# Optimization experiments

Hardware: AMD Instinct MI355X
Metric: run time of the kernel (lower is better)

The kernel has to match this reference:

```python
import jax, jax.numpy as jnp
import numpy as np

NEG_SLOPE = 0.2  # PyG GATConv default negative_slope
EPS = 1e-16


def gat_conv(x, edge_index, W, att_src, att_dst, bias, heads, out_c, concat):
    """Faithful PyG GATConv forward (add_self_loops=True).
    x: [N, F_in], edge_index: [2, E] (row 0 = src, row 1 = dst),
    W: [heads*out_c, F_in], att_src/att_dst: [1, heads, out_c], bias: [out]
    """
    N = x.shape[0]
    loop = jnp.arange(N, dtype=edge_index.dtype)
    src = jnp.concatenate([edge_index[0], loop])
    dst = jnp.concatenate([edge_index[1], loop])

    h = (x @ W.T).reshape(N, heads, out_c)            # [N, H, C]
    a_src = jnp.sum(h * att_src, axis=-1)             # [N, H]
    a_dst = jnp.sum(h * att_dst, axis=-1)             # [N, H]

    e = jax.nn.leaky_relu(a_src[src] + a_dst[dst], NEG_SLOPE)   # [E+N, H]
    # numerically-stable segment softmax over incoming edges of dst
    m = jax.ops.segment_max(e, dst, num_segments=N)             # [N, H]
    p = jnp.exp(e - m[dst])
    denom = jax.ops.segment_sum(p, dst, num_segments=N)         # [N, H]
    alpha = p / (denom[dst] + EPS)                              # [E+N, H]

    out = jax.ops.segment_sum(h[src] * alpha[:, :, None], dst, num_segments=N)  # [N, H, C]
    out = out.reshape(N, heads * out_c) if concat else out.mean(axis=1)
    return out + bias


def setup_inputs() -> dict:
    key = jax.random.key(0)
    ks = jax.random.split(key, 11)
    N, E = 100_000, 1_600_000
    in_dim, hid, heads = 128, 64, 2
    s = 0.1
    x = jax.random.normal(ks[0], (N, in_dim), jnp.float32)
    edge_index_l2 = jax.random.randint(ks[1], (2, E), 0, N, dtype=jnp.int32)
    edge_index_l1 = jax.random.randint(ks[2], (2, E), 0, N, dtype=jnp.int32)
    # layer gat_l2: in_dim -> hid per head, heads=2, concat=True
    W2 = jax.random.normal(ks[3], (heads * hid, in_dim), jnp.float32) * s
    att_src2 = jax.random.normal(ks[4], (1, heads, hid), jnp.float32) * s
    att_dst2 = jax.random.normal(ks[5], (1, heads, hid), jnp.float32) * s
    b2 = jnp.zeros((heads * hid,), jnp.float32)
    # layer gat_l1: hid*heads -> hid, 1 head, concat=False
    W1 = jax.random.normal(ks[6], (hid, heads * hid), jnp.float32) * s
    att_src1 = jax.random.normal(ks[7], (1, 1, hid), jnp.float32) * s
    att_dst1 = jax.random.normal(ks[8], (1, 1, hid), jnp.float32) * s
    b1 = jnp.zeros((hid,), jnp.float32)
    return {
        "x": x,
        "edge_index_l1": edge_index_l1,
        "edge_index_l2": edge_index_l2,
        "W2": W2, "att_src2": att_src2, "att_dst2": att_dst2, "b2": b2,
        "W1": W1, "att_src1": att_src1, "att_dst1": att_dst1, "b1": b1,
    }


def reference(x, edge_index_l1, edge_index_l2, W2, att_src2, att_dst2, b2,
              W1, att_src1, att_dst1, b1):
    h = jax.nn.elu(gat_conv(x, edge_index_l2, W2, att_src2, att_dst2, b2,
                            heads=2, out_c=64, concat=True))    # [N, 128]
    h = jax.nn.elu(gat_conv(h, edge_index_l1, W1, att_src1, att_dst1, b1,
                            heads=1, out_c=64, concat=False))   # [N, 64]
    return h
```

## Files before the change

kernel.cpp:

```cpp
#include <hip/hip_runtime.h>
#include <hip/hip_bf16.h>
#include <math.h>

#define LRELU_SLOPE 0.2f
#define EPS 1e-16f
#define BUCK_SHIFT 8
#define BUCK_NODES 256
#define MAXBUCK 512

typedef __hip_bfloat16 bf16;
typedef __attribute__((ext_vector_type(8))) short bf16x8;
typedef __attribute__((ext_vector_type(4))) float f32x4;

__device__ inline float lrelu(float v) { return v > 0.f ? v : LRELU_SLOPE * v; }
__device__ inline float bflo(unsigned u) { return __uint_as_float(u << 16); }
__device__ inline float bfhi(unsigned u) { return __uint_as_float(u & 0xffff0000u); }
__device__ inline short f2bf(float f) {
  bf16 t = __float2bfloat16(f);
  return *reinterpret_cast<short*>(&t);
}
__device__ inline unsigned pack2(float lo, float hi) {
  return ((unsigned)(unsigned short)f2bf(hi) << 16) | (unsigned)(unsigned short)f2bf(lo);
}

__global__ void prep_kernel(const float* __restrict__ W2, unsigned short* __restrict__ Wb2,
                            const float* __restrict__ W1, unsigned short* __restrict__ Wb1,
                            int* __restrict__ gcur, int ngc) {
  int idx = blockIdx.x * blockDim.x + threadIdx.x;
  if (idx < ngc) gcur[idx] = 0;
  if (idx < 16384) {
    Wb2[idx] = (unsigned short)f2bf(W2[idx]);
  } else {
    int i = idx - 16384;
    if (i < 8192) Wb1[i] = (unsigned short)f2bf(W1[i]);
  }
}

template <int EPB>
__global__ __launch_bounds__(256) void partition_both_kernel(
    const int* __restrict__ ei2, int E2, int* __restrict__ gcur2, int* __restrict__ slab2,
    const int* __restrict__ ei1, int E1, int* __restrict__ gcur1, int* __restrict__ slab1,
    int cap, int nbuck, int nblk2) {
  __shared__ int cnt[MAXBUCK];
  __shared__ int sbase[MAXBUCK];
  const int tid = threadIdx.x;
  const bool l2 = (int)blockIdx.x < nblk2;
  const int bid = l2 ? blockIdx.x : blockIdx.x - nblk2;
  const int* ei = l2 ? ei2 : ei1;
  const int E = l2 ? E2 : E1;
  int* gcur = l2 ? gcur2 : gcur1;
  int* part = l2 ? slab2 : slab1;
  for (int t = tid; t < nbuck; t += 256) cnt[t] = 0;
  __syncthreads();
  const int e0 = bid * EPB;
  constexpr int KPT = EPB / 256;
  int sv[KPT], dv[KPT];
#pragma unroll
  for (int k = 0; k < KPT; k++) {
    int e = e0 + tid + k * 256;
    if (e < E) {
      sv[k] = ei[e];
      dv[k] = ei[E + e];
      atomicAdd(&cnt[dv[k] >> BUCK_SHIFT], 1);
    } else {
      dv[k] = -1;
    }
  }
  __syncthreads();
  for (int t = tid; t < nbuck; t += 256) {
    int c = cnt[t];
    if (c) sbase[t] = atomicAdd(&gcur[t], c);
    cnt[t] = 0;
  }
  __syncthreads();
#pragma unroll
  for (int k = 0; k < KPT; k++) {
    if (dv[k] >= 0) {
      int b = dv[k] >> BUCK_SHIFT;
      int pos = sbase[b] + atomicAdd(&cnt[b], 1);
      if (pos < cap) part[(size_t)b * cap + pos] = (sv[k] << 8) | (dv[k] & (BUCK_NODES - 1));
    }
  }
}

template <int H>
__global__ __launch_bounds__(256) void csr_build_kernel(
    int* __restrict__ slab, const int* __restrict__ gcur, int cap,
    const float* __restrict__ asrc, const float* __restrict__ adst, float* __restrict__ pcsr,
    int* __restrict__ rowbeg, int* __restrict__ rowend, int N) {
  extern __shared__ char smem[];
  int* s_sd = (int*)smem;
  int* hist = (int*)(s_sd + cap);
  int* histp = hist + 256;
  int* escanp = histp + 256;
  int* cur = escanp + 256;
  int* wtot = cur + 256;
  float* s_ad = (float*)(wtot + 4);

  const int b = blockIdx.x;
  const int tid = threadIdx.x;
  const int lane = tid & 63;
  const int wid = tid >> 6;
  const int nb0 = b << BUCK_SHIFT;
  const int nn = min(BUCK_NODES, N - nb0);
  const int cnt = min(gcur[b], cap - 7 * BUCK_NODES);
  const int B = b * cap;
  int* eidx = slab;

  hist[tid] = 0;
  cur[tid] = 0;
  for (int t = tid; t < nn * H; t += 256) s_ad[t] = adst[(size_t)nb0 * H + t];
  __syncthreads();
  for (int i = tid; i < cnt; i += 256) {
    int pr = slab[(size_t)B + i];
    s_sd[i] = pr;
    atomicAdd(&hist[pr & (BUCK_NODES - 1)], 1);
  }
  __syncthreads();
  const int h0 = hist[tid];
  const int hp = (h0 + 7) & ~7;
  histp[tid] = hp;
  int inc = hp;
#pragma unroll
  for (int off = 1; off < 64; off <<= 1) {
    int t = __shfl_up(inc, off);
    if (lane >= off) inc += t;
  }
  if (lane == 63) wtot[wid] = inc;
  __syncthreads();
  int base = 0;
  for (int w = 0; w < wid; w++) base += wtot[w];
  escanp[tid] = inc + base;
  if (tid < nn) {
    rowbeg[nb0 + tid] = B + inc + base - hp;
    rowend[nb0 + tid] = B + inc + base;
  }
  __syncthreads();
  for (int i = tid; i < cnt; i += 256) {
    int pr = s_sd[i];
    int d8 = pr & (BUCK_NODES - 1);
    int s = pr >> 8;
    int slot = B + (escanp[d8] - histp[d8]) + atomicAdd(&cur[d8], 1);
    eidx[slot] = s;
    if constexpr (H == 2) {
      float2 a = *(const float2*)&asrc[2 * (size_t)s];
      float2 ad = *(const float2*)&s_ad[2 * d8];
      float2 pv;
      pv.x = __expf(lrelu(a.x + ad.x));
      pv.y = __expf(lrelu(a.y + ad.y));
      *(float2*)&pcsr[2 * (size_t)slot] = pv;
    } else {
      pcsr[slot] = __expf(lrelu(asrc[s] + s_ad[d8]));
    }
  }
  if (tid < nn) {
    int pb = B + escanp[tid] - histp[tid];
    for (int k = h0; k < hp; k++) {
      eidx[pb + k] = nb0 + tid;
      if constexpr (H == 2) {
        *(float2*)&pcsr[2 * (size_t)(pb + k)] = make_float2(0.f, 0.f);
      } else {
        pcsr[pb + k] = 0.f;
      }
    }
  }
}

template <int M, int H, bool SPLIT, typename Tin>
__global__ __launch_bounds__(256) void gemm_att_mfma(
    const Tin* __restrict__ x, const unsigned short* __restrict__ Wb,
    const float* __restrict__ atts, const float* __restrict__ attd, bf16* __restrict__ h,
    float* __restrict__ asrc, float* __restrict__ adst, float* __restrict__ pself, int N) {
  constexpr int K = 128;
  constexpr int NF = M / 16;
  const int wid = threadIdx.x >> 6;
  const int lane = threadIdx.x & 63;
  const int r0 = blockIdx.x * 64 + wid * 16;
  if (r0 >= N) return;
  const int colb = lane & 15;
  const int kgrp = lane >> 4;
  const size_t arow = (size_t)min(r0 + colb, N - 1);

  f32x4 acc[NF];
#pragma unroll
  for (int f = 0; f < NF; f++) acc[f] = (f32x4){0.f, 0.f, 0.f, 0.f};

#pragma unroll
  for (int k0 = 0; k0 < K; k0 += 32) {
    const int kb = k0 + kgrp * 8;
    bf16x8 ahi, alo;
    if constexpr (SPLIT) {
      const float* xp = (const float*)x + arow * K + kb;
      float4 l0 = *(const float4*)xp;
      float4 l1 = *(const float4*)(xp + 4);
      float xv[8] = {l0.x, l0.y, l0.z, l0.w, l1.x, l1.y, l1.z, l1.w};
#pragma unroll
      for (int j = 0; j < 8; j++) {
        short hb = f2bf(xv[j]);
        ahi[j] = hb;
        float hf = __uint_as_float(((unsigned)(unsigned short)hb) << 16);
        alo[j] = f2bf(xv[j] - hf);
      }
    } else {
      ahi = *(const bf16x8*)((const unsigned short*)x + arow * K + kb);
    }
#pragma unroll
    for (int f = 0; f < NF; f++) {
      bf16x8 b = *(const bf16x8*)(Wb + (size_t)(f * 16 + colb) * K + kb);
      if constexpr (SPLIT)
        acc[f] = __builtin_amdgcn_mfma_f32_16x16x32_bf16(alo, b, acc[f], 0, 0, 0);
      acc[f] = __builtin_amdgcn_mfma_f32_16x16x32_bf16(ahi, b, acc[f], 0, 0, 0);
    }
  }

#pragma unroll
  for (int r = 0; r < 4; r++) {
    const int row = r0 + kgrp * 4 + r;
    const bool ok = row < N;
    float s0 = 0.f, d0 = 0.f, s1 = 0.f, d1 = 0.f;
#pragma unroll
    for (int f = 0; f < NF; f++) {
      float v = acc[f][r];
      int c = f * 16 + colb;
      if (ok) h[(size_t)row * M + c] = __float2bfloat16(v);
      float av = atts[c], dv = attd[c];
      if (H == 2 && f >= NF / 2) {
        s1 += v * av;
        d1 += v * dv;
      } else {
        s0 += v * av;
        d0 += v * dv;
      }
    }
#pragma unroll
    for (int off = 1; off < 16; off <<= 1) {
      s0 += __shfl_xor(s0, off);
      d0 += __shfl_xor(d0, off);
      if (H == 2) {
        s1 += __shfl_xor(s1, off);
        d1 += __shfl_xor(d1, off);
      }
    }
    if (ok && colb == 0) {
      if (H == 2) {
        asrc[2 * (size_t)row] = s0;
        asrc[2 * (size_t)row + 1] = s1;
        adst[2 * (size_t)row] = d0;
        adst[2 * (size_t)row + 1] = d1;
        *(float2*)&pself[2 * (size_t)row] =
            make_float2(__expf(lrelu(s0 + d0)), __expf(lrelu(s1 + d1)));
      } else {
        asrc[row] = s0;
        adst[row] = d0;
        pself[row] = __expf(lrelu(s0 + d0));
      }
    }
  }
}

__global__ void gather2_kernel(const bf16* __restrict__ h, const float* __restrict__ pself,
                               const int* __restrict__ rowbeg, const int* __restrict__ rowend,
                               const int* __restrict__ eidx, const float* __restrict__ pcsr,
                               const float* __restrict__ bias, bf16* __restrict__ outp, int N) {
  long long gt = (long long)blockIdx.x * blockDim.x + threadIdx.x;
  int n = (int)(gt >> 6);
  int lane = threadIdx.x & 63;
  if (n >= N) return;
  const int qw = lane >> 4;
  const int cl = lane & 15;
  const bool head0 = cl < 8;
  int start = rowbeg[n];
  int end = rowend[n];
  const float2 ps = *(const float2*)&pself[2 * (size_t)n];
  float g = qw ? 0.f : (head0 ? ps.x : ps.y);
  uint4 hv = *(const uint4*)&h[(size_t)n * 128 + 8 * cl];
  float den = g;
  float a0 = g * bflo(hv.x), a1 = g * bfhi(hv.x);
  float a2 = g * bflo(hv.y), a3 = g * bfhi(hv.y);
  float a4 = g * bflo(hv.z), a5 = g * bfhi(hv.z);
  float a6 = g * bflo(hv.w), a7 = g * bfhi(hv.w);
  for (int j = start + 4 * qw; j < end; j += 16) {
    int4 ia = *(const int4*)&eidx[j];
    float4 q0 = *(const float4*)&pcsr[2 * (size_t)j];
    float4 q1 = *(const float4*)&pcsr[2 * (size_t)j + 4];
    uint4 hA = *(const uint4*)&h[(size_t)ia.x * 128 + 8 * cl];
    uint4 hB = *(const uint4*)&h[(size_t)ia.y * 128 + 8 * cl];
    uint4 hC = *(const uint4*)&h[(size_t)ia.z * 128 + 8 * cl];
    uint4 hD = *(const uint4*)&h[(size_t)ia.w * 128 + 8 * cl];
    float pa = head0 ? q0.x : q0.y;
    float pb = head0 ? q0.z : q0.w;
    float pc = head0 ? q1.x : q1.y;
    float pd = head0 ? q1.z : q1.w;
    den += (pa + pb) + (pc + pd);
    a0 += (pa * bflo(hA.x) + pb * bflo(hB.x)) + (pc * bflo(hC.x) + pd * bflo(hD.x));
    a1 += (pa * bfhi(hA.x) + pb * bfhi(hB.x)) + (pc * bfhi(hC.x) + pd * bfhi(hD.x));
    a2 += (pa * bflo(hA.y) + pb * bflo(hB.y)) + (pc * bflo(hC.y) + pd * bflo(hD.y));
    a3 += (pa * bfhi(hA.y) + pb * bfhi(hB.y)) + (pc * bfhi(hC.y) + pd * bfhi(hD.y));
    a4 += (pa * bflo(hA.z) + pb * bflo(hB.z)) + (pc * bflo(hC.z) + pd * bflo(hD.z));
    a5 += (pa * bfhi(hA.z) + pb * bfhi(hB.z)) + (pc * bfhi(hC.z) + pd * bfhi(hD.z));
    a6 += (pa * bflo(hA.w) + pb * bflo(hB.w)) + (pc * bflo(hC.w) + pd * bflo(hD.w));
    a7 += (pa * bfhi(hA.w) + pb * bfhi(hB.w)) + (pc * bfhi(hC.w) + pd * bfhi(hD.w));
  }
#pragma unroll
  for (int off = 16; off <= 32; off <<= 1) {
    den += __shfl_xor(den, off);
    a0 += __shfl_xor(a0, off);
    a1 += __shfl_xor(a1, off);
    a2 += __shfl_xor(a2, off);
    a3 += __shfl_xor(a3, off);
    a4 += __shfl_xor(a4, off);
    a5 += __shfl_xor(a5, off);
    a6 += __shfl_xor(a6, off);
    a7 += __shfl_xor(a7, off);
  }
  if (qw == 0) {
    float rden = 1.f / (den + EPS);
    float4 bv0 = *(const float4*)&bias[8 * cl];
    float4 bv1 = *(const float4*)&bias[8 * cl + 4];
    float v0 = a0 * rden + bv0.x;
    float v1 = a1 * rden + bv0.y;
    float v2 = a2 * rden + bv0.z;
    float v3 = a3 * rden + bv0.w;
    float v4 = a4 * rden + bv1.x;
    float v5 = a5 * rden + bv1.y;
    float v6 = a6 * rden + bv1.z;
    float v7 = a7 * rden + bv1.w;
    v0 = v0 > 0.f ? v0 : expm1f(v0);
    v1 = v1 > 0.f ? v1 : expm1f(v1);
    v2 = v2 > 0.f ? v2 : expm1f(v2);
    v3 = v3 > 0.f ? v3 : expm1f(v3);
    v4 = v4 > 0.f ? v4 : expm1f(v4);
    v5 = v5 > 0.f ? v5 : expm1f(v5);
    v6 = v6 > 0.f ? v6 : expm1f(v6);
    v7 = v7 > 0.f ? v7 : expm1f(v7);
    uint4 o;
    o.x = pack2(v0, v1);
    o.y = pack2(v2, v3);
    o.z = pack2(v4, v5);
    o.w = pack2(v6, v7);
    *(uint4*)&outp[(size_t)n * 128 + 8 * cl] = o;
  }
}

__global__ void gather1_kernel(const bf16* __restrict__ h, const float* __restrict__ pself,
                               const int* __restrict__ rowbeg, const int* __restrict__ rowend,
                               const int* __restrict__ eidx, const float* __restrict__ pcsr,
                               const float* __restrict__ bias, float* __restrict__ outp, int N) {
  long long gt = (long long)blockIdx.x * blockDim.x + threadIdx.x;
  int n = (int)(gt >> 6);
  int lane = threadIdx.x & 63;
  if (n >= N) return;
  const int qw = lane >> 4;
  const int cl = lane & 15;
  int start = rowbeg[n];
  int end = rowend[n];
  uint2 hv = *(const uint2*)&h[(size_t)n * 64 + 4 * cl];
  float g = qw ? 0.f : pself[n];
  float den = g;
  float a0 = g * bflo(hv.x), a1 = g * bfhi(hv.x);
  float a2 = g * bflo(hv.y), a3 = g * bfhi(hv.y);
  for (int j = start + 4 * qw; j < end; j += 16) {
    int4 ia = *(const int4*)&eidx[j];
    float4 pv = *(const float4*)&pcsr[j];
    uint2 hA = *(const uint2*)&h[(size_t)ia.x * 64 + 4 * cl];
    uint2 hB = *(const uint2*)&h[(size_t)ia.y * 64 + 4 * cl];
    uint2 hC = *(const uint2*)&h[(size_t)ia.z * 64 + 4 * cl];
    uint2 hD = *(const uint2*)&h[(size_t)ia.w * 64 + 4 * cl];
    den += (pv.x + pv.y) + (pv.z + pv.w);
    a0 += (pv.x * bflo(hA.x) + pv.y * bflo(hB.x)) + (pv.z * bflo(hC.x) + pv.w * bflo(hD.x));
    a1 += (pv.x * bfhi(hA.x) + pv.y * bfhi(hB.x)) + (pv.z * bfhi(hC.x) + pv.w * bfhi(hD.x));
    a2 += (pv.x * bflo(hA.y) + pv.y * bflo(hB.y)) + (pv.z * bflo(hC.y) + pv.w * bflo(hD.y));
    a3 += (pv.x * bfhi(hA.y) + pv.y * bfhi(hB.y)) + (pv.z * bfhi(hC.y) + pv.w * bfhi(hD.y));
  }
#pragma unroll
  for (int off = 16; off <= 32; off <<= 1) {
    den += __shfl_xor(den, off);
    a0 += __shfl_xor(a0, off);
    a1 += __shfl_xor(a1, off);
    a2 += __shfl_xor(a2, off);
    a3 += __shfl_xor(a3, off);
  }
  if (qw == 0) {
    float rden = 1.f / (den + EPS);
    float4 bv = *(const float4*)&bias[4 * cl];
    float v0 = a0 * rden + bv.x;
    float v1 = a1 * rden + bv.y;
    float v2 = a2 * rden + bv.z;
    float v3 = a3 * rden + bv.w;
    v0 = v0 > 0.f ? v0 : expm1f(v0);
    v1 = v1 > 0.f ? v1 : expm1f(v1);
    v2 = v2 > 0.f ? v2 : expm1f(v2);
    v3 = v3 > 0.f ? v3 : expm1f(v3);
    *(float4*)&outp[(size_t)n * 64 + 4 * cl] = make_float4(v0, v1, v2, v3);
  }
}

extern "C" void kernel_launch(void* const* d_in, const int* in_sizes, int n_in,
                              void* d_out, int out_size, void* d_ws, size_t ws_size,
                              hipStream_t stream) {
  const float* x = (const float*)d_in[0];
  const int* ei1 = (const int*)d_in[1];
  const int* ei2 = (const int*)d_in[2];
  const float* W2 = (const float*)d_in[3];
  const float* as2 = (const float*)d_in[4];
  const float* ad2 = (const float*)d_in[5];
  const float* b2 = (const float*)d_in[6];
  const float* W1 = (const float*)d_in[7];
  const float* as1 = (const float*)d_in[8];
  const float* ad1 = (const float*)d_in[9];
  const float* b1 = (const float*)d_in[10];
  float* out = (float*)d_out;

  const int N = in_sizes[0] / 128;
  const int E1 = in_sizes[1] / 2;
  const int E2 = in_sizes[2] / 2;
  const int Emax = E1 > E2 ? E1 : E2;
  const size_t Ns = (size_t)N;

  const int nbuck = (N + BUCK_NODES - 1) / BUCK_NODES;
  int lam = (Emax + nbuck - 1) / nbuck;
  int cap = lam + (lam >> 2) + 2048;
  cap = (cap + 255) & ~(int)255;
  const size_t NC = (size_t)nbuck * cap;

  float* ws = (float*)d_ws;
  size_t o = 0;
  unsigned short* Wb2 = (unsigned short*)(ws + o); o += 8192;
  unsigned short* Wb1 = (unsigned short*)(ws + o); o += 4096;
  float* asrc2 = ws + o;  o += 2 * Ns;
  float* adst2 = ws + o;  o += 2 * Ns;
  float* pself2 = ws + o; o += 2 * Ns;
  float* asrc1 = ws + o;  o += Ns;
  float* adst1 = ws + o;  o += Ns;
  float* pself1 = ws + o; o += Ns;
  int* gcur2 = (int*)(ws + o);   o += (size_t)nbuck;
  int* gcur1 = (int*)(ws + o);   o += (size_t)nbuck;
  int* rowbeg2 = (int*)(ws + o); o += Ns;
  int* rowend2 = (int*)(ws + o); o += Ns;
  int* rowbeg1 = (int*)(ws + o); o += Ns;
  int* rowend1 = (int*)(ws + o); o += Ns;
  o = (o + 7) & ~(size_t)7;
  int* slab2 = (int*)(ws + o);   o += NC;
  int* slab1 = (int*)(ws + o);   o += NC;
  o = (o + 7) & ~(size_t)7;
  float* pcsr = ws + o;          o += 2 * NC;
  o = (o + 7) & ~(size_t)7;
  bf16* h2 = (bf16*)(ws + o);    o += 64 * Ns;
  bf16* h1 = h2;
  bf16* hin1 = (bf16*)(ws + o);  o += 64 * Ns;

  const size_t smem2 = (size_t)cap * 4 + 4 * 256 * 4 + 16 + 2 * 256 * 4 + 64;
  const size_t smem1 = (size_t)cap * 4 + 4 * 256 * 4 + 16 + 1 * 256 * 4 + 64;

  const int nblk2 = (E2 + 4095) / 4096;
  const int nblk1 = (E1 + 4095) / 4096;

  prep_kernel<<<(16384 + 8192 + 255) / 256, 256, 0, stream>>>(W2, Wb2, W1, Wb1, gcur2, 2 * nbuck);
  partition_both_kernel<4096><<<nblk2 + nblk1, 256, 0, stream>>>(
      ei2, E2, gcur2, slab2, ei1, E1, gcur1, slab1, cap, nbuck, nblk2);

  gemm_att_mfma<128, 2, true, float>
      <<<(N + 63) / 64, 256, 0, stream>>>(x, Wb2, as2, ad2, h2, asrc2, adst2, pself2, N);
  csr_build_kernel<2><<<nbuck, 256, smem2, stream>>>(slab2, gcur2, cap, asrc2, adst2, pcsr,
                                                     rowbeg2, rowend2, N);
  gather2_kernel<<<(N + 3) / 4, 256, 0, stream>>>(h2, pself2, rowbeg2, rowend2, slab2, pcsr,
                                                  b2, hin1, N);

  gemm_att_mfma<64, 1, false, bf16>
      <<<(N + 63) / 64, 256, 0, stream>>>(hin1, Wb1, as1, ad1, h1, asrc1, adst1, pself1, N);
  csr_build_kernel<1><<<nbuck, 256, smem1, stream>>>(slab1, gcur1, cap, asrc1, adst1, pcsr,
                                                     rowbeg1, rowend1, N);
  gather1_kernel<<<(N + 3) / 4, 256, 0, stream>>>(h1, pself1, rowbeg1, rowend1, slab1, pcsr,
                                                  b1, out, N);
}
```

Baseline: 315.2 us.

## Fuse CSR build with neighbor gather per bucket and halve bucket size

The separate CSR-build and gather kernels of each layer are merged into one kernel per bucket. After sorting its bucket's edges in shared memory, each block aggregates its own nodes, reading row offsets from the shared scan instead of global rowbeg/rowend arrays. Buckets shrink from 256 to 128 nodes, giving more blocks and a smaller per-bucket slab, and the capacity slack is tightened. This removes two launches and the rowbeg/rowend round trip, and keeps freshly written eidx/pcsr hot in cache. In exchange, gather parallelism drops to a few hundred blocks, each wave processing 32 nodes serially, which may weaken latency hiding for the random feature loads.

```diff
diff --git a/kernel.cpp b/kernel.cpp
--- a/kernel.cpp
+++ b/kernel.cpp
@@ -4,9 +4,9 @@
 
 #define LRELU_SLOPE 0.2f
 #define EPS 1e-16f
-#define BUCK_SHIFT 8
-#define BUCK_NODES 256
-#define MAXBUCK 512
+#define BUCK_SHIFT 7
+#define BUCK_NODES 128
+#define MAXBUCK 1024
 
 typedef __hip_bfloat16 bf16;
 typedef __attribute__((ext_vector_type(8))) short bf16x8;
@@ -78,90 +78,7 @@
     if (dv[k] >= 0) {
       int b = dv[k] >> BUCK_SHIFT;
       int pos = sbase[b] + atomicAdd(&cnt[b], 1);
-      if (pos < cap) part[(size_t)b * cap + pos] = (sv[k] << 8) | (dv[k] & (BUCK_NODES - 1));
-    }
-  }
-}
-
-template <int H>
-__global__ __launch_bounds__(256) void csr_build_kernel(
-    int* __restrict__ slab, const int* __restrict__ gcur, int cap,
-    const float* __restrict__ asrc, const float* __restrict__ adst, float* __restrict__ pcsr,
-    int* __restrict__ rowbeg, int* __restrict__ rowend, int N) {
-  extern __shared__ char smem[];
-  int* s_sd = (int*)smem;
-  int* hist = (int*)(s_sd + cap);
-  int* histp = hist + 256;
-  int* escanp = histp + 256;
-  int* cur = escanp + 256;
-  int* wtot = cur + 256;
-  float* s_ad = (float*)(wtot + 4);
-
-  const int b = blockIdx.x;
-  const int tid = threadIdx.x;
-  const int lane = tid & 63;
-  const int wid = tid >> 6;
-  const int nb0 = b << BUCK_SHIFT;
-  const int nn = min(BUCK_NODES, N - nb0);
-  const int cnt = min(gcur[b], cap - 7 * BUCK_NODES);
-  const int B = b * cap;
-  int* eidx = slab;
-
-  hist[tid] = 0;
-  cur[tid] = 0;
-  for (int t = tid; t < nn * H; t += 256) s_ad[t] = adst[(size_t)nb0 * H + t];
-  __syncthreads();
-  for (int i = tid; i < cnt; i += 256) {
-    int pr = slab[(size_t)B + i];
-    s_sd[i] = pr;
-    atomicAdd(&hist[pr & (BUCK_NODES - 1)], 1);
-  }
-  __syncthreads();
-  const int h0 = hist[tid];
-  const int hp = (h0 + 7) & ~7;
-  histp[tid] = hp;
-  int inc = hp;
-#pragma unroll
-  for (int off = 1; off < 64; off <<= 1) {
-    int t = __shfl_up(inc, off);
-    if (lane >= off) inc += t;
-  }
-  if (lane == 63) wtot[wid] = inc;
-  __syncthreads();
-  int base = 0;
-  for (int w = 0; w < wid; w++) base += wtot[w];
-  escanp[tid] = inc + base;
-  if (tid < nn) {
-    rowbeg[nb0 + tid] = B + inc + base - hp;
-    rowend[nb0 + tid] = B + inc + base;
-  }
-  __syncthreads();
-  for (int i = tid; i < cnt; i += 256) {
-    int pr = s_sd[i];
-    int d8 = pr & (BUCK_NODES - 1);
-    int s = pr >> 8;
-    int slot = B + (escanp[d8] - histp[d8]) + atomicAdd(&cur[d8], 1);
-    eidx[slot] = s;
-    if constexpr (H == 2) {
-      float2 a = *(const float2*)&asrc[2 * (size_t)s];
-      float2 ad = *(const float2*)&s_ad[2 * d8];
-      float2 pv;
-      pv.x = __expf(lrelu(a.x + ad.x));
-      pv.y = __expf(lrelu(a.y + ad.y));
-      *(float2*)&pcsr[2 * (size_t)slot] = pv;
-    } else {
-      pcsr[slot] = __expf(lrelu(asrc[s] + s_ad[d8]));
-    }
-  }
-  if (tid < nn) {
-    int pb = B + escanp[tid] - histp[tid];
-    for (int k = h0; k < hp; k++) {
-      eidx[pb + k] = nb0 + tid;
-      if constexpr (H == 2) {
-        *(float2*)&pcsr[2 * (size_t)(pb + k)] = make_float2(0.f, 0.f);
-      } else {
-        pcsr[pb + k] = 0.f;
-      }
+      if (pos < cap) part[(size_t)b * cap + pos] = (sv[k] << BUCK_SHIFT) | (dv[k] & (BUCK_NODES - 1));
     }
   }
 }
@@ -258,140 +175,209 @@
   }
 }
 
-__global__ void gather2_kernel(const bf16* __restrict__ h, const float* __restrict__ pself,
-                               const int* __restrict__ rowbeg, const int* __restrict__ rowend,
-                               const int* __restrict__ eidx, const float* __restrict__ pcsr,
-                               const float* __restrict__ bias, bf16* __restrict__ outp, int N) {
-  long long gt = (long long)blockIdx.x * blockDim.x + threadIdx.x;
-  int n = (int)(gt >> 6);
-  int lane = threadIdx.x & 63;
-  if (n >= N) return;
+template <int H, typename TOut>
+__global__ __launch_bounds__(256) void csr_gather_kernel(
+    int* __restrict__ slab, const int* __restrict__ gcur, int cap,
+    const float* __restrict__ asrc, const float* __restrict__ adst,
+    const float* __restrict__ pself, float* __restrict__ pcsr, const bf16* __restrict__ h,
+    const float* __restrict__ bias, TOut* __restrict__ outp, int N) {
+  extern __shared__ char smem[];
+  int* s_sd = (int*)smem;
+  int* hist = (int*)(s_sd + cap);
+  int* histp = hist + 256;
+  int* escanp = histp + 256;
+  int* cur = escanp + 256;
+  int* wtot = cur + 256;
+  float* s_ad = (float*)(wtot + 4);
+
+  const int b = blockIdx.x;
+  const int tid = threadIdx.x;
+  const int lane = tid & 63;
+  const int wid = tid >> 6;
+  const int nb0 = b << BUCK_SHIFT;
+  const int nn = min(BUCK_NODES, N - nb0);
+  const int cnt = min(gcur[b], cap - 7 * BUCK_NODES);
+  const int B = b * cap;
+  int* eidx = slab;
+
+  hist[tid] = 0;
+  cur[tid] = 0;
+  for (int t = tid; t < nn * H; t += 256) s_ad[t] = adst[(size_t)nb0 * H + t];
+  __syncthreads();
+  for (int i = tid; i < cnt; i += 256) {
+    int pr = slab[(size_t)B + i];
+    s_sd[i] = pr;
+    atomicAdd(&hist[pr & (BUCK_NODES - 1)], 1);
+  }
+  __syncthreads();
+  const int h0 = hist[tid];
+  const int hp = (h0 + 7) & ~7;
+  histp[tid] = hp;
+  int inc = hp;
+#pragma unroll
+  for (int off = 1; off < 64; off <<= 1) {
+    int t = __shfl_up(inc, off);
+    if (lane >= off) inc += t;
+  }
+  if (lane == 63) wtot[wid] = inc;
+  __syncthreads();
+  int base = 0;
+  for (int w = 0; w < wid; w++) base += wtot[w];
+  escanp[tid] = inc + base;
+  __syncthreads();
+  for (int i = tid; i < cnt; i += 256) {
+    int pr = s_sd[i];
+    int d7 = pr & (BUCK_NODES - 1);
+    int s = pr >> BUCK_SHIFT;
+    int slot = B + (escanp[d7] - histp[d7]) + atomicAdd(&cur[d7], 1);
+    eidx[slot] = s;
+    if constexpr (H == 2) {
+      float2 a = *(const float2*)&asrc[2 * (size_t)s];
+      float2 ad = *(const float2*)&s_ad[2 * d7];
+      float2 pv;
+      pv.x = __expf(lrelu(a.x + ad.x));
+      pv.y = __expf(lrelu(a.y + ad.y));
+      *(float2*)&pcsr[2 * (size_t)slot] = pv;
+    } else {
+      pcsr[slot] = __expf(lrelu(asrc[s] + s_ad[d7]));
+    }
+  }
+  if (tid < nn) {
+    int pb = B + escanp[tid] - histp[tid];
+    for (int k = h0; k < hp; k++) {
+      eidx[pb + k] = nb0 + tid;
+      if constexpr (H == 2) {
+        *(float2*)&pcsr[2 * (size_t)(pb + k)] = make_float2(0.f, 0.f);
+      } else {
+        pcsr[pb + k] = 0.f;
+      }
+    }
+  }
+  __syncthreads();
+
   const int qw = lane >> 4;
   const int cl = lane & 15;
-  const bool head0 = cl < 8;
-  int start = rowbeg[n];
-  int end = rowend[n];
-  const float2 ps = *(const float2*)&pself[2 * (size_t)n];
-  float g = qw ? 0.f : (head0 ? ps.x : ps.y);
-  uint4 hv = *(const uint4*)&h[(size_t)n * 128 + 8 * cl];
-  float den = g;
-  float a0 = g * bflo(hv.x), a1 = g * bfhi(hv.x);
-  float a2 = g * bflo(hv.y), a3 = g * bfhi(hv.y);
-  float a4 = g * bflo(hv.z), a5 = g * bfhi(hv.z);
-  float a6 = g * bflo(hv.w), a7 = g * bfhi(hv.w);
-  for (int j = start + 4 * qw; j < end; j += 16) {
-    int4 ia = *(const int4*)&eidx[j];
-    float4 q0 = *(const float4*)&pcsr[2 * (size_t)j];
-    float4 q1 = *(const float4*)&pcsr[2 * (size_t)j + 4];
-    uint4 hA = *(const uint4*)&h[(size_t)ia.x * 128 + 8 * cl];
-    uint4 hB = *(const uint4*)&h[(size_t)ia.y * 128 + 8 * cl];
-    uint4 hC = *(const uint4*)&h[(size_t)ia.z * 128 + 8 * cl];
-    uint4 hD = *(const uint4*)&h[(size_t)ia.w * 128 + 8 * cl];
-    float pa = head0 ? q0.x : q0.y;
-    float pb = head0 ? q0.z : q0.w;
-    float pc = head0 ? q1.x : q1.y;
-    float pd = head0 ? q1.z : q1.w;
-    den += (pa + pb) + (pc + pd);
-    a0 += (pa * bflo(hA.x) + pb * bflo(hB.x)) + (pc * bflo(hC.x) + pd * bflo(hD.x));
-    a1 += (pa * bfhi(hA.x) + pb * bfhi(hB.x)) + (pc * bfhi(hC.x) + pd * bfhi(hD.x));
-    a2 += (pa * bflo(hA.y) + pb * bflo(hB.y)) + (pc * bflo(hC.y) + pd * bflo(hD.y));
-    a3 += (pa * bfhi(hA.y) + pb * bfhi(hB.y)) + (pc * bfhi(hC.y) + pd * bfhi(hD.y));
-    a4 += (pa * bflo(hA.z) + pb * bflo(hB.z)) + (pc * bflo(hC.z) + pd * bflo(hD.z));
-    a5 += (pa * bfhi(hA.z) + pb * bfhi(hB.z)) + (pc * bfhi(hC.z) + pd * bfhi(hD.z));
-    a6 += (pa * bflo(hA.w) + pb * bflo(hB.w)) + (pc * bflo(hC.w) + pd * bflo(hD.w));
-    a7 += (pa * bfhi(hA.w) + pb * bfhi(hB.w)) + (pc * bfhi(hC.w) + pd * bfhi(hD.w));
-  }
-#pragma unroll
-  for (int off = 16; off <= 32; off <<= 1) {
-    den += __shfl_xor(den, off);
-    a0 += __shfl_xor(a0, off);
-    a1 += __shfl_xor(a1, off);
-    a2 += __shfl_xor(a2, off);
-    a3 += __shfl_xor(a3, off);
-    a4 += __shfl_xor(a4, off);
-    a5 += __shfl_xor(a5, off);
-    a6 += __shfl_xor(a6, off);
-    a7 += __shfl_xor(a7, off);
-  }
-  if (qw == 0) {
-    float rden = 1.f / (den + EPS);
-    float4 bv0 = *(const float4*)&bias[8 * cl];
-    float4 bv1 = *(const float4*)&bias[8 * cl + 4];
-    float v0 = a0 * rden + bv0.x;
-    float v1 = a1 * rden + bv0.y;
-    float v2 = a2 * rden + bv0.z;
-    float v3 = a3 * rden + bv0.w;
-    float v4 = a4 * rden + bv1.x;
-    float v5 = a5 * rden + bv1.y;
-    float v6 = a6 * rden + bv1.z;
-    float v7 = a7 * rden + bv1.w;
-    v0 = v0 > 0.f ? v0 : expm1f(v0);
-    v1 = v1 > 0.f ? v1 : expm1f(v1);
-    v2 = v2 > 0.f ? v2 : expm1f(v2);
-    v3 = v3 > 0.f ? v3 : expm1f(v3);
-    v4 = v4 > 0.f ? v4 : expm1f(v4);
-    v5 = v5 > 0.f ? v5 : expm1f(v5);
-    v6 = v6 > 0.f ? v6 : expm1f(v6);
-    v7 = v7 > 0.f ? v7 : expm1f(v7);
-    uint4 o;
-    o.x = pack2(v0, v1);
-    o.y = pack2(v2, v3);
-    o.z = pack2(v4, v5);
-    o.w = pack2(v6, v7);
-    *(uint4*)&outp[(size_t)n * 128 + 8 * cl] = o;
-  }
-}
-
-__global__ void gather1_kernel(const bf16* __restrict__ h, const float* __restrict__ pself,
-                               const int* __restrict__ rowbeg, const int* __restrict__ rowend,
-                               const int* __restrict__ eidx, const float* __restrict__ pcsr,
-                               const float* __restrict__ bias, float* __restrict__ outp, int N) {
-  long long gt = (long long)blockIdx.x * blockDim.x + threadIdx.x;
-  int n = (int)(gt >> 6);
-  int lane = threadIdx.x & 63;
-  if (n >= N) return;
-  const int qw = lane >> 4;
-  const int cl = lane & 15;
-  int start = rowbeg[n];
-  int end = rowend[n];
-  uint2 hv = *(const uint2*)&h[(size_t)n * 64 + 4 * cl];
-  float g = qw ? 0.f : pself[n];
-  float den = g;
-  float a0 = g * bflo(hv.x), a1 = g * bfhi(hv.x);
-  float a2 = g * bflo(hv.y), a3 = g * bfhi(hv.y);
-  for (int j = start + 4 * qw; j < end; j += 16) {
-    int4 ia = *(const int4*)&eidx[j];
-    float4 pv = *(const float4*)&pcsr[j];
-    uint2 hA = *(const uint2*)&h[(size_t)ia.x * 64 + 4 * cl];
-    uint2 hB = *(const uint2*)&h[(size_t)ia.y * 64 + 4 * cl];
-    uint2 hC = *(const uint2*)&h[(size_t)ia.z * 64 + 4 * cl];
-    uint2 hD = *(const uint2*)&h[(size_t)ia.w * 64 + 4 * cl];
-    den += (pv.x + pv.y) + (pv.z + pv.w);
-    a0 += (pv.x * bflo(hA.x) + pv.y * bflo(hB.x)) + (pv.z * bflo(hC.x) + pv.w * bflo(hD.x));
-    a1 += (pv.x * bfhi(hA.x) + pv.y * bfhi(hB.x)) + (pv.z * bfhi(hC.x) + pv.w * bfhi(hD.x));
-    a2 += (pv.x * bflo(hA.y) + pv.y * bflo(hB.y)) + (pv.z * bflo(hC.y) + pv.w * bflo(hD.y));
-    a3 += (pv.x * bfhi(hA.y) + pv.y * bfhi(hB.y)) + (pv.z * bfhi(hC.y) + pv.w * bfhi(hD.y));
-  }
-#pragma unroll
-  for (int off = 16; off <= 32; off <<= 1) {
-    den += __shfl_xor(den, off);
-    a0 += __shfl_xor(a0, off);
-    a1 += __shfl_xor(a1, off);
-    a2 += __shfl_xor(a2, off);
-    a3 += __shfl_xor(a3, off);
-  }
-  if (qw == 0) {
-    float rden = 1.f / (den + EPS);
-    float4 bv = *(const float4*)&bias[4 * cl];
-    float v0 = a0 * rden + bv.x;
-    float v1 = a1 * rden + bv.y;
-    float v2 = a2 * rden + bv.z;
-    float v3 = a3 * rden + bv.w;
-    v0 = v0 > 0.f ? v0 : expm1f(v0);
-    v1 = v1 > 0.f ? v1 : expm1f(v1);
-    v2 = v2 > 0.f ? v2 : expm1f(v2);
-    v3 = v3 > 0.f ? v3 : expm1f(v3);
-    *(float4*)&outp[(size_t)n * 64 + 4 * cl] = make_float4(v0, v1, v2, v3);
+  if constexpr (H == 2) {
+    const bool head0 = cl < 8;
+    for (int ln = wid; ln < nn; ln += 4) {
+      const int n = nb0 + ln;
+      const int start = B + escanp[ln] - histp[ln];
+      const int end = B + escanp[ln];
+      const float2 ps = *(const float2*)&pself[2 * (size_t)n];
+      float g = qw ? 0.f : (head0 ? ps.x : ps.y);
+      uint4 hv = *(const uint4*)&h[(size_t)n * 128 + 8 * cl];
+      float den = g;
+      float a0 = g * bflo(hv.x), a1 = g * bfhi(hv.x);
+      float a2 = g * bflo(hv.y), a3 = g * bfhi(hv.y);
+      float a4 = g * bflo(hv.z), a5 = g * bfhi(hv.z);
+      float a6 = g * bflo(hv.w), a7 = g * bfhi(hv.w);
+      for (int j = start + 4 * qw; j < end; j += 16) {
+        int4 ia = *(const int4*)&eidx[j];
+        float4 q0 = *(const float4*)&pcsr[2 * (size_t)j];
+        float4 q1 = *(const float4*)&pcsr[2 * (size_t)j + 4];
+        uint4 hA = *(const uint4*)&h[(size_t)ia.x * 128 + 8 * cl];
+        uint4 hB = *(const uint4*)&h[(size_t)ia.y * 128 + 8 * cl];
+        uint4 hC = *(const uint4*)&h[(size_t)ia.z * 128 + 8 * cl];
+        uint4 hD = *(const uint4*)&h[(size_t)ia.w * 128 + 8 * cl];
+        float pa = head0 ? q0.x : q0.y;
+        float pb = head0 ? q0.z : q0.w;
+        float pc = head0 ? q1.x : q1.y;
+        float pd = head0 ? q1.z : q1.w;
+        den += (pa + pb) + (pc + pd);
+        a0 += (pa * bflo(hA.x) + pb * bflo(hB.x)) + (pc * bflo(hC.x) + pd * bflo(hD.x));
+        a1 += (pa * bfhi(hA.x) + pb * bfhi(hB.x)) + (pc * bfhi(hC.x) + pd * bfhi(hD.x));
+        a2 += (pa * bflo(hA.y) + pb * bflo(hB.y)) + (pc * bflo(hC.y) + pd * bflo(hD.y));
+        a3 += (pa * bfhi(hA.y) + pb * bfhi(hB.y)) + (pc * bfhi(hC.y) + pd * bfhi(hD.y));
+        a4 += (pa * bflo(hA.z) + pb * bflo(hB.z)) + (pc * bflo(hC.z) + pd * bflo(hD.z));
+        a5 += (pa * bfhi(hA.z) + pb * bfhi(hB.z)) + (pc * bfhi(hC.z) + pd * bfhi(hD.z));
+        a6 += (pa * bflo(hA.w) + pb * bflo(hB.w)) + (pc * bflo(hC.w) + pd * bflo(hD.w));
+        a7 += (pa * bfhi(hA.w) + pb * bfhi(hB.w)) + (pc * bfhi(hC.w) + pd * bfhi(hD.w));
+      }
+#pragma unroll
+      for (int off = 16; off <= 32; off <<= 1) {
+        den += __shfl_xor(den, off);
+        a0 += __shfl_xor(a0, off);
+        a1 += __shfl_xor(a1, off);
+        a2 += __shfl_xor(a2, off);
+        a3 += __shfl_xor(a3, off);
+        a4 += __shfl_xor(a4, off);
+        a5 += __shfl_xor(a5, off);
+        a6 += __shfl_xor(a6, off);
+        a7 += __shfl_xor(a7, off);
+      }
+      if (qw == 0) {
+        float rden = 1.f / (den + EPS);
+        float4 bv0 = *(const float4*)&bias[8 * cl];
+        float4 bv1 = *(const float4*)&bias[8 * cl + 4];
+        float v0 = a0 * rden + bv0.x;
+        float v1 = a1 * rden + bv0.y;
+        float v2 = a2 * rden + bv0.z;
+        float v3 = a3 * rden + bv0.w;
+        float v4 = a4 * rden + bv1.x;
+        float v5 = a5 * rden + bv1.y;
+        float v6 = a6 * rden + bv1.z;
+        float v7 = a7 * rden + bv1.w;
+        v0 = v0 > 0.f ? v0 : expm1f(v0);
+        v1 = v1 > 0.f ? v1 : expm1f(v1);
+        v2 = v2 > 0.f ? v2 : expm1f(v2);
+        v3 = v3 > 0.f ? v3 : expm1f(v3);
+        v4 = v4 > 0.f ? v4 : expm1f(v4);
+        v5 = v5 > 0.f ? v5 : expm1f(v5);
+        v6 = v6 > 0.f ? v6 : expm1f(v6);
+        v7 = v7 > 0.f ? v7 : expm1f(v7);
+        uint4 o;
+        o.x = pack2(v0, v1);
+        o.y = pack2(v2, v3);
+        o.z = pack2(v4, v5);
+        o.w = pack2(v6, v7);
+        *(uint4*)&((bf16*)outp)[(size_t)n * 128 + 8 * cl] = o;
+      }
+    }
+  } else {
+    for (int ln = wid; ln < nn; ln += 4) {
+      const int n = nb0 + ln;
+      const int start = B + escanp[ln] - histp[ln];
+      const int end = B + escanp[ln];
+      uint2 hv = *(const uint2*)&h[(size_t)n * 64 + 4 * cl];
+      float g = qw ? 0.f : pself[n];
+      float den = g;
+      float a0 = g * bflo(hv.x), a1 = g * bfhi(hv.x);
+      float a2 = g * bflo(hv.y), a3 = g * bfhi(hv.y);
+      for (int j = start + 4 * qw; j < end; j += 16) {
+        int4 ia = *(const int4*)&eidx[j];
+        float4 pv = *(const float4*)&pcsr[j];
+        uint2 hA = *(const uint2*)&h[(size_t)ia.x * 64 + 4 * cl];
+        uint2 hB = *(const uint2*)&h[(size_t)ia.y * 64 + 4 * cl];
+        uint2 hC = *(const uint2*)&h[(size_t)ia.z * 64 + 4 * cl];
+        uint2 hD = *(const uint2*)&h[(size_t)ia.w * 64 + 4 * cl];
+        den += (pv.x + pv.y) + (pv.z + pv.w);
+        a0 += (pv.x * bflo(hA.x) + pv.y * bflo(hB.x)) + (pv.z * bflo(hC.x) + pv.w * bflo(hD.x));
+        a1 += (pv.x * bfhi(hA.x) + pv.y * bfhi(hB.x)) + (pv.z * bfhi(hC.x) + pv.w * bfhi(hD.x));
+        a2 += (pv.x * bflo(hA.y) + pv.y * bflo(hB.y)) + (pv.z * bflo(hC.y) + pv.w * bflo(hD.y));
+        a3 += (pv.x * bfhi(hA.y) + pv.y * bfhi(hB.y)) + (pv.z * bfhi(hC.y) + pv.w * bfhi(hD.y));
+      }
+#pragma unroll
+      for (int off = 16; off <= 32; off <<= 1) {
+        den += __shfl_xor(den, off);
+        a0 += __shfl_xor(a0, off);
+        a1 += __shfl_xor(a1, off);
+        a2 += __shfl_xor(a2, off);
+        a3 += __shfl_xor(a3, off);
+      }
+      if (qw == 0) {
+        float rden = 1.f / (den + EPS);
+        float4 bv = *(const float4*)&bias[4 * cl];
+        float v0 = a0 * rden + bv.x;
+        float v1 = a1 * rden + bv.y;
+        float v2 = a2 * rden + bv.z;
+        float v3 = a3 * rden + bv.w;
+        v0 = v0 > 0.f ? v0 : expm1f(v0);
+        v1 = v1 > 0.f ? v1 : expm1f(v1);
+        v2 = v2 > 0.f ? v2 : expm1f(v2);
+        v3 = v3 > 0.f ? v3 : expm1f(v3);
+        *(float4*)&((float*)outp)[(size_t)n * 64 + 4 * cl] = make_float4(v0, v1, v2, v3);
+      }
+    }
   }
 }
 
@@ -419,8 +405,8 @@
 
   const int nbuck = (N + BUCK_NODES - 1) / BUCK_NODES;
   int lam = (Emax + nbuck - 1) / nbuck;
-  int cap = lam + (lam >> 2) + 2048;
-  cap = (cap + 255) & ~(int)255;
+  int cap = lam + (lam >> 3) + 1408;
+  cap = (cap + 63) & ~(int)63;
   const size_t NC = (size_t)nbuck * cap;
 
   float* ws = (float*)d_ws;
@@ -435,10 +421,6 @@
   float* pself1 = ws + o; o += Ns;
   int* gcur2 = (int*)(ws + o);   o += (size_t)nbuck;
   int* gcur1 = (int*)(ws + o);   o += (size_t)nbuck;
-  int* rowbeg2 = (int*)(ws + o); o += Ns;
-  int* rowend2 = (int*)(ws + o); o += Ns;
-  int* rowbeg1 = (int*)(ws + o); o += Ns;
-  int* rowend1 = (int*)(ws + o); o += Ns;
   o = (o + 7) & ~(size_t)7;
   int* slab2 = (int*)(ws + o);   o += NC;
   int* slab1 = (int*)(ws + o);   o += NC;
@@ -449,8 +431,8 @@
   bf16* h1 = h2;
   bf16* hin1 = (bf16*)(ws + o);  o += 64 * Ns;
 
-  const size_t smem2 = (size_t)cap * 4 + 4 * 256 * 4 + 16 + 2 * 256 * 4 + 64;
-  const size_t smem1 = (size_t)cap * 4 + 4 * 256 * 4 + 16 + 1 * 256 * 4 + 64;
+  const size_t smem2 = (size_t)cap * 4 + 4 * 256 * 4 + 16 + 2 * BUCK_NODES * 4 + 64;
+  const size_t smem1 = (size_t)cap * 4 + 4 * 256 * 4 + 16 + 1 * BUCK_NODES * 4 + 64;
 
   const int nblk2 = (E2 + 4095) / 4096;
   const int nblk1 = (E1 + 4095) / 4096;
@@ -461,15 +443,11 @@
 
   gemm_att_mfma<128, 2, true, float>
       <<<(N + 63) / 64, 256, 0, stream>>>(x, Wb2, as2, ad2, h2, asrc2, adst2, pself2, N);
-  csr_build_kernel<2><<<nbuck, 256, smem2, stream>>>(slab2, gcur2, cap, asrc2, adst2, pcsr,
-                                                     rowbeg2, rowend2, N);
-  gather2_kernel<<<(N + 3) / 4, 256, 0, stream>>>(h2, pself2, rowbeg2, rowend2, slab2, pcsr,
-                                                  b2, hin1, N);
+  csr_gather_kernel<2, bf16><<<nbuck, 256, smem2, stream>>>(
+      slab2, gcur2, cap, asrc2, adst2, pself2, pcsr, h2, b2, hin1, N);
 
   gemm_att_mfma<64, 1, false, bf16>
       <<<(N + 63) / 64, 256, 0, stream>>>(hin1, Wb1, as1, ad1, h1, asrc1, adst1, pself1, N);
-  csr_build_kernel<1><<<nbuck, 256, smem1, stream>>>(slab1, gcur1, cap, asrc1, adst1, pcsr,
-                                                     rowbeg1, rowend1, N);
-  gather1_kernel<<<(N + 3) / 4, 256, 0, stream>>>(h1, pself1, rowbeg1, rowend1, slab1, pcsr,
-                                                  b1, out, N);
-}
+  csr_gather_kernel<1, float><<<nbuck, 256, smem1, stream>>>(
+      slab1, gcur1, cap, asrc1, adst1, pself1, pcsr, h1, b1, out, N);
+}
```

After: 360.8 us. 1.14x slower.
